# Performance work log

Measured on AMD Instinct MI355X. Metric: run time of the kernel, lower is better.

Reference implementation:

```python
import jax, jax.numpy as jnp
import numpy as np

B, T, C = 256, 2048, 64
WINDOW_RATIO = 0.1
SCALES = (0.5, 2.0)
WARP_SIZE = int(np.ceil(WINDOW_RATIO * T))            # 205, matches np.ceil(...).astype(int)
L_MAX = (T - WARP_SIZE) + int(WARP_SIZE * max(SCALES))  # max warped length (scale=2.0) = 2253


def setup_inputs() -> dict:
    key = jax.random.key(0)
    k1, k2, k3 = jax.random.split(key, 3)
    x = jax.random.normal(k1, (B, T, C), dtype=jnp.float32)
    # np.random.choice(scales, B)
    warp_scales = jnp.asarray(SCALES, jnp.float32)[jax.random.randint(k2, (B,), 0, len(SCALES))]
    # np.random.randint(low=1, high=T - warp_size - 1, size=B)
    window_starts = jax.random.randint(k3, (B,), 1, T - WARP_SIZE - 1).astype(jnp.int32)
    return {"x": x, "warp_scales": warp_scales, "window_starts": window_starts}


def _lerp_gather(arr, pos, max_idx):
    # arr: [B, L, C]; pos: [B, N] fractional indices -> [B, N, C] linear interp
    p0 = jnp.floor(pos)
    frac = (pos - p0)[..., None]
    i0 = p0.astype(jnp.int32)
    i1 = jnp.minimum(i0 + 1, max_idx)
    g0 = jnp.take_along_axis(arr, i0[..., None], axis=1)
    g1 = jnp.take_along_axis(arr, i1[..., None], axis=1)
    return g0 * (1.0 - frac) + g1 * frac


def _window_warp(x, warp_scales, window_starts):
    Bx, Tx, Cx = x.shape
    # int(warp_size * scale): truncation == floor for positive values
    new_len = jnp.floor(WARP_SIZE * warp_scales)          # [B] float, resampled window length
    L = (Tx - WARP_SIZE) + new_len                        # [B] float, total warped length per sample
    start = window_starts.astype(x.dtype)[:, None]        # [B,1]
    nl = new_len[:, None]                                 # [B,1]

    # Stage 1: build warped sequence of padded length L_MAX via fractional gather from x.
    # warped[j] = x[j]                       for j < start
    #           = interp(x window) at s_win  for start <= j < start+new_len
    #           = x[j - new_len + warp_size] for j >= start+new_len (garbage past L, never read)
    j = jnp.arange(L_MAX, dtype=x.dtype)[None, :]         # [1, L_MAX]
    in_win = (j >= start) & (j < start + nl)
    after = j >= start + nl
    s_win = start + (j - start) * (WARP_SIZE - 1) / jnp.maximum(nl - 1.0, 1.0)
    s = jnp.where(in_win, s_win, jnp.where(after, j - nl + WARP_SIZE, j))
    s = jnp.clip(s, 0.0, Tx - 1)
    warped = _lerp_gather(x, s, Tx - 1)                   # [B, L_MAX, C]

    # Stage 2: np.interp(arange(T), linspace(0, T-1, L), warped) == linear interp of
    # warped at fractional index u = t * (L-1) / (T-1)
    t = jnp.arange(Tx, dtype=x.dtype)[None, :]            # [1, T]
    u = t * (L[:, None] - 1.0) / (Tx - 1.0)
    u = jnp.clip(u, 0.0, L[:, None] - 1.0)
    return _lerp_gather(warped, u, L_MAX - 1)             # [B, T, C]


def reference(x, warp_scales, window_starts):
    return _window_warp(x, warp_scales, window_starts)
```

## Files before the change

kernel.cpp:

```cpp
#include <hip/hip_runtime.h>
#include <stdint.h>

constexpr int Bn     = 256;
constexpr int Tn     = 2048;
constexpr int Cn     = 64;
constexpr int WARPSZ = 205;
constexpr int LMAX   = 2253;

constexpr int TB = 32;
constexpr int NR = 72;

typedef float f32x4 __attribute__((ext_vector_type(4)));

__device__ __forceinline__ void map_j(float jf, float start, float nl, float rdenom,
                                      int& i0, int& i1, float& fr) {
    bool in_win = (jf >= start) && (jf < start + nl);
    bool after  = (jf >= start + nl);
    float s_win   = start + (jf - start) * rdenom;
    float s_after = jf - nl + (float)WARPSZ;
    float s = in_win ? s_win : (after ? s_after : jf);
    s = fminf(fmaxf(s, 0.0f), (float)(Tn - 1));
    float p0 = floorf(s);
    fr = s - p0;
    i0 = (int)p0;
    i1 = min(i0 + 1, Tn - 1);
}

__global__ __launch_bounds__(256) void window_warp_kernel(
        const float* __restrict__ x,
        const float* __restrict__ scales,
        const int*   __restrict__ starts,
        float*       __restrict__ out) {
    __shared__ f32x4 smem[NR * (Cn / 4)];

    int n    = blockIdx.x;
    int bidx = ((n & 7) << 11) | (n >> 3);
    int b     = bidx >> 6;
    int t0    = (bidx & 63) << 5;
    int tslot = threadIdx.x >> 4;
    int cg    = threadIdx.x & 15;

    float scale = scales[b];
    float start = (float)starts[b];
    float nl    = floorf((float)WARPSZ * scale);
    float Lm1   = (float)(Tn - WARPSZ) + nl - 1.0f;
    float rdenom = (float)(WARPSZ - 1) / fmaxf(nl - 1.0f, 1.0f);

    float u0 = ((float)t0 * Lm1) / (float)(Tn - 1);
    u0 = fminf(fmaxf(u0, 0.0f), Lm1);
    int j00 = (int)floorf(u0);
    int r0a, r0b; float fr0;
    map_j((float)j00, start, nl, rdenom, r0a, r0b, fr0);
    int rbase = min(r0a, Tn - NR);

    {
        const float* gbase = x + (size_t)b * (Tn * Cn) + rbase * Cn;
        int wave = threadIdx.x >> 6;
        int lane = threadIdx.x & 63;
        float* sm = (float*)smem;
        #pragma unroll
        for (int c = wave; c < (NR * Cn * 4) / 1024; c += 4) {
            __builtin_amdgcn_global_load_lds(
                (const __attribute__((address_space(1))) uint32_t*)(gbase + c * 256 + lane * 4),
                (__attribute__((address_space(3))) uint32_t*)(sm + c * 256),
                16, 0, 0);
        }
    }
    __syncthreads();

    int   i00[2], i01[2], i10[2], i11[2];
    float f0[2], f1[2], fu[2];
    #pragma unroll
    for (int k = 0; k < 2; ++k) {
        int t = t0 + tslot + 16 * k;
        float u = ((float)t * Lm1) / (float)(Tn - 1);
        u = fminf(fmaxf(u, 0.0f), Lm1);
        float q0 = floorf(u);
        fu[k] = u - q0;
        int j0 = (int)q0;
        int j1 = min(j0 + 1, LMAX - 1);
        map_j((float)j0, start, nl, rdenom, i00[k], i01[k], f0[k]);
        map_j((float)j1, start, nl, rdenom, i10[k], i11[k], f1[k]);
    }

    f32x4 A0[2], A1[2], B0[2], B1[2];
    #pragma unroll
    for (int k = 0; k < 2; ++k) {
        A0[k] = smem[(i00[k] - rbase) * 16 + cg];
        A1[k] = smem[(i01[k] - rbase) * 16 + cg];
        B0[k] = smem[(i10[k] - rbase) * 16 + cg];
        B1[k] = smem[(i11[k] - rbase) * 16 + cg];
    }

    f32x4* outb = (f32x4*)(out + (size_t)b * (Tn * Cn));
    #pragma unroll
    for (int k = 0; k < 2; ++k) {
        int t = t0 + tslot + 16 * k;
        float g0 = 1.0f - f0[k], g1 = 1.0f - f1[k], gu = 1.0f - fu[k];
        f32x4 v0 = A0[k] * g0 + A1[k] * f0[k];
        f32x4 v1 = B0[k] * g1 + B1[k] * f1[k];
        f32x4 r  = v0 * gu + v1 * fu[k];
        __builtin_nontemporal_store(r, &outb[t * 16 + cg]);
    }
}

extern "C" void kernel_launch(void* const* d_in, const int* in_sizes, int n_in,
                              void* d_out, int out_size, void* d_ws, size_t ws_size,
                              hipStream_t stream) {
    const float* x      = (const float*)d_in[0];
    const float* scales = (const float*)d_in[1];
    const int*   starts = (const int*)d_in[2];
    float* out = (float*)d_out;

    int blocks = Bn * Tn / TB;
    window_warp_kernel<<<blocks, 256, 0, stream>>>(x, scales, starts, out);
}
```

Baseline: 237.5 us.

## Process eight time tiles per block with double-buffered async LDS staging

```diff
diff --git a/kernel.cpp b/kernel.cpp
--- a/kernel.cpp
+++ b/kernel.cpp
@@ -7,8 +7,9 @@
 constexpr int WARPSZ = 205;
 constexpr int LMAX   = 2253;
 
-constexpr int TB = 32;
-constexpr int NR = 72;
+constexpr int TB     = 32;
+constexpr int NR     = 80;
+constexpr int NTILES = 8;
 
 typedef float f32x4 __attribute__((ext_vector_type(4)));
 
@@ -31,14 +32,16 @@
         const float* __restrict__ scales,
         const int*   __restrict__ starts,
         float*       __restrict__ out) {
-    __shared__ f32x4 smem[NR * (Cn / 4)];
+    __shared__ f32x4 smem[2][NR * (Cn / 4)];
 
-    int n    = blockIdx.x;
-    int bidx = ((n & 7) << 11) | (n >> 3);
-    int b     = bidx >> 6;
-    int t0    = (bidx & 63) << 5;
+    int n       = blockIdx.x;
+    int logical = ((n & 7) << 8) | (n >> 3);
+    int b        = logical >> 3;
+    int t_origin = (logical & 7) << 8;
     int tslot = threadIdx.x >> 4;
     int cg    = threadIdx.x & 15;
+    int wave  = threadIdx.x >> 6;
+    int lane  = threadIdx.x & 63;
 
     float scale = scales[b];
     float start = (float)starts[b];
@@ -46,61 +49,84 @@
     float Lm1   = (float)(Tn - WARPSZ) + nl - 1.0f;
     float rdenom = (float)(WARPSZ - 1) / fmaxf(nl - 1.0f, 1.0f);
 
-    float u0 = ((float)t0 * Lm1) / (float)(Tn - 1);
-    u0 = fminf(fmaxf(u0, 0.0f), Lm1);
-    int j00 = (int)floorf(u0);
-    int r0a, r0b; float fr0;
-    map_j((float)j00, start, nl, rdenom, r0a, r0b, fr0);
-    int rbase = min(r0a, Tn - NR);
+    const float* xb   = x + (size_t)b * (Tn * Cn);
+    f32x4*       outb = (f32x4*)(out + (size_t)b * (Tn * Cn));
 
-    {
-        const float* gbase = x + (size_t)b * (Tn * Cn) + rbase * Cn;
-        int wave = threadIdx.x >> 6;
-        int lane = threadIdx.x & 63;
-        float* sm = (float*)smem;
+    int rb[NTILES];
+    #pragma unroll
+    for (int tau = 0; tau < NTILES; ++tau) {
+        int t0 = t_origin + tau * TB;
+        float u0 = ((float)t0 * Lm1) / (float)(Tn - 1);
+        u0 = fminf(fmaxf(u0, 0.0f), Lm1);
+        int j00 = (int)floorf(u0);
+        int ra, rx; float fr;
+        map_j((float)j00, start, nl, rdenom, ra, rx, fr);
+        rb[tau] = min(ra, Tn - NR);
+    }
+
+    auto STAGE = [&](int bufidx, int rbase) {
+        const float* gb = xb + rbase * Cn;
+        float* sm = (float*)&smem[bufidx][0];
         #pragma unroll
-        for (int c = wave; c < (NR * Cn * 4) / 1024; c += 4) {
+        for (int j = 0; j < 5; ++j) {
+            int c = wave + 4 * j;
             __builtin_amdgcn_global_load_lds(
-                (const __attribute__((address_space(1))) uint32_t*)(gbase + c * 256 + lane * 4),
+                (const __attribute__((address_space(1))) uint32_t*)(gb + c * 256 + lane * 4),
                 (__attribute__((address_space(3))) uint32_t*)(sm + c * 256),
                 16, 0, 0);
         }
-    }
-    __syncthreads();
+    };
 
-    int   i00[2], i01[2], i10[2], i11[2];
-    float f0[2], f1[2], fu[2];
+    auto COMPUTE = [&](int bufidx, int t0, int rbase) {
+        int   i00[2], i01[2], i10[2], i11[2];
+        float f0[2], f1[2], fu[2];
+        #pragma unroll
+        for (int k = 0; k < 2; ++k) {
+            int t = t0 + tslot + 16 * k;
+            float u = ((float)t * Lm1) / (float)(Tn - 1);
+            u = fminf(fmaxf(u, 0.0f), Lm1);
+            float q0 = floorf(u);
+            fu[k] = u - q0;
+            int j0 = (int)q0;
+            int j1 = min(j0 + 1, LMAX - 1);
+            map_j((float)j0, start, nl, rdenom, i00[k], i01[k], f0[k]);
+            map_j((float)j1, start, nl, rdenom, i10[k], i11[k], f1[k]);
+        }
+        const f32x4* sm = &smem[bufidx][0];
+        f32x4 A0[2], A1[2], B0[2], B1[2];
+        #pragma unroll
+        for (int k = 0; k < 2; ++k) {
+            A0[k] = sm[(i00[k] - rbase) * 16 + cg];
+            A1[k] = sm[(i01[k] - rbase) * 16 + cg];
+            B0[k] = sm[(i10[k] - rbase) * 16 + cg];
+            B1[k] = sm[(i11[k] - rbase) * 16 + cg];
+        }
+        #pragma unroll
+        for (int k = 0; k < 2; ++k) {
+            int t = t0 + tslot + 16 * k;
+            float g0 = 1.0f - f0[k], g1 = 1.0f - f1[k], gu = 1.0f - fu[k];
+            f32x4 v0 = A0[k] * g0 + A1[k] * f0[k];
+            f32x4 v1 = B0[k] * g1 + B1[k] * f1[k];
+            f32x4 r  = v0 * gu + v1 * fu[k];
+            __builtin_nontemporal_store(r, (f32x4*)&outb[t * 16 + cg]);
+        }
+    };
+
+    STAGE(0, rb[0]);
     #pragma unroll
-    for (int k = 0; k < 2; ++k) {
-        int t = t0 + tslot + 16 * k;
-        float u = ((float)t * Lm1) / (float)(Tn - 1);
-        u = fminf(fmaxf(u, 0.0f), Lm1);
-        float q0 = floorf(u);
-        fu[k] = u - q0;
-        int j0 = (int)q0;
-        int j1 = min(j0 + 1, LMAX - 1);
-        map_j((float)j0, start, nl, rdenom, i00[k], i01[k], f0[k]);
-        map_j((float)j1, start, nl, rdenom, i10[k], i11[k], f1[k]);
-    }
-
-    f32x4 A0[2], A1[2], B0[2], B1[2];
-    #pragma unroll
-    for (int k = 0; k < 2; ++k) {
-        A0[k] = smem[(i00[k] - rbase) * 16 + cg];
-        A1[k] = smem[(i01[k] - rbase) * 16 + cg];
-        B0[k] = smem[(i10[k] - rbase) * 16 + cg];
-        B1[k] = smem[(i11[k] - rbase) * 16 + cg];
-    }
-
-    f32x4* outb = (f32x4*)(out + (size_t)b * (Tn * Cn));
-    #pragma unroll
-    for (int k = 0; k < 2; ++k) {
-        int t = t0 + tslot + 16 * k;
-        float g0 = 1.0f - f0[k], g1 = 1.0f - f1[k], gu = 1.0f - fu[k];
-        f32x4 v0 = A0[k] * g0 + A1[k] * f0[k];
-        f32x4 v1 = B0[k] * g1 + B1[k] * f1[k];
-        f32x4 r  = v0 * gu + v1 * fu[k];
-        __builtin_nontemporal_store(r, &outb[t * 16 + cg]);
+    for (int tau = 0; tau < NTILES; ++tau) {
+        if (tau >= 1)
+            __builtin_amdgcn_s_barrier();
+        if (tau + 1 < NTILES)
+            STAGE((tau + 1) & 1, rb[tau + 1]);
+        if (tau == 0)
+            asm volatile("s_waitcnt vmcnt(5)" ::: "memory");
+        else if (tau + 1 < NTILES)
+            asm volatile("s_waitcnt vmcnt(7)" ::: "memory");
+        else
+            asm volatile("s_waitcnt vmcnt(2)" ::: "memory");
+        __builtin_amdgcn_s_barrier();
+        COMPUTE(tau & 1, t_origin + tau * TB, rb[tau]);
     }
 }
 
@@ -112,6 +138,6 @@
     const int*   starts = (const int*)d_in[2];
     float* out = (float*)d_out;
 
-    int blocks = Bn * Tn / TB;
+    int blocks = Bn * Tn / (TB * NTILES);
     window_warp_kernel<<<blocks, 256, 0, stream>>>(x, scales, starts, out);
 }
```

Measured after the change: 246.6 us. +3.8%, slower.
